# Performance work log

Hardware: AMD Instinct MI355X
Metric: run time of the kernel (lower is better)

## Reference

```python
import jax, jax.numpy as jnp
import numpy as np

N_HEADS, N_LEVELS, N_POINTS = 8, 4, 4
D_MODEL, UNIT = 384, 128

@jax.custom_vjp
def grl(x):
    # Gradient Reversal Layer: identity forward, -grad backward (lambda_=1)
    return x

def _grl_fwd(x):
    return x, None

def _grl_bwd(res, g):
    return (-g,)

grl.defvjp(_grl_fwd, _grl_bwd)


def ms_deform_attn_core(value, spatial_shapes_np, loc, attn):
    """Multi-scale deformable attention (grid_sample bilinear, zeros padding, align_corners=False).
    value: (N, Len_in, nH, hd)   loc: (N, Lq, nH, nL, nP, 2) normalized [0,1]   attn: (N, Lq, nH, nL, nP)
    """
    N, Lq, nH, nL, nP, _ = loc.shape
    hd = value.shape[-1]
    b = jnp.arange(N).reshape(N, 1, 1, 1)
    h = jnp.arange(nH).reshape(1, 1, nH, 1)
    out = jnp.zeros((N, Lq, nH, hd), dtype=value.dtype)
    start = 0
    for l in range(nL):
        H, W = int(spatial_shapes_np[l, 0]), int(spatial_shapes_np[l, 1])
        v = value[:, start:start + H * W]  # (N, H*W, nH, hd)
        start += H * W
        # align_corners=False pixel coords
        x = loc[:, :, :, l, :, 0] * W - 0.5
        y = loc[:, :, :, l, :, 1] * H - 0.5
        x0f, y0f = jnp.floor(x), jnp.floor(y)
        lx, ly = x - x0f, y - y0f
        x0, y0 = x0f.astype(jnp.int32), y0f.astype(jnp.int32)
        def gather(xi, yi):
            valid = ((xi >= 0) & (xi < W) & (yi >= 0) & (yi < H)).astype(value.dtype)
            flat = jnp.clip(yi, 0, H - 1) * W + jnp.clip(xi, 0, W - 1)  # (N,Lq,nH,nP)
            return v[b, flat, h] * valid[..., None]  # (N,Lq,nH,nP,hd)
        s = (((1 - lx) * (1 - ly))[..., None] * gather(x0, y0)
             + (lx * (1 - ly))[..., None] * gather(x0 + 1, y0)
             + ((1 - lx) * ly)[..., None] * gather(x0, y0 + 1)
             + (lx * ly)[..., None] * gather(x0 + 1, y0 + 1))
        out = out + jnp.sum(s * attn[:, :, :, l, :, None], axis=3)
    return out.reshape(N, Lq, nH * hd)


def setup_inputs() -> dict:
    key = jax.random.key(0)
    ks = jax.random.split(key, 12)
    N, Lq = 2, 5440
    spatial = np.array([[64, 64], [32, 32], [16, 16], [8, 8]], dtype=np.int32)
    sizes = spatial[:, 0] * spatial[:, 1]
    Len_in = int(sizes.sum())  # 5440
    lsi = np.concatenate([[0], np.cumsum(sizes)[:-1]]).astype(np.int32)
    D, U, nH, nL, nP = D_MODEL, UNIT, N_HEADS, N_LEVELS, N_POINTS
    def lin(k, fin, fout):
        return jax.random.normal(k, (fin, fout), jnp.float32) / np.sqrt(fin)
    # faithful grid-init bias for sampling offsets
    thetas = np.arange(nH) * (2.0 * np.pi / nH)
    grid = np.stack([np.cos(thetas), np.sin(thetas)], -1)
    grid = grid / np.abs(grid).max(-1, keepdims=True)
    grid = np.tile(grid.reshape(nH, 1, 1, 2), (1, nL, nP, 1))
    for i in range(nP):
        grid[:, :, i, :] *= (i + 1)
    return {
        "query": jax.random.normal(ks[0], (N, Lq, D), jnp.float32),
        "reference_points": jax.random.uniform(ks[1], (N, Lq, nL, 2), jnp.float32),
        "input_flatten": jax.random.normal(ks[2], (N, Len_in, D), jnp.float32),
        "input_spatial_shapes": jnp.asarray(spatial),
        "input_level_start_index": jnp.asarray(lsi),
        "W_off": 0.01 * jax.random.normal(ks[3], (2 * U, nH * nL * nP * 2), jnp.float32),
        "b_off": jnp.asarray(grid.reshape(-1), dtype=jnp.float32),
        "W_attn": lin(ks[4], 2 * U, nH * nL * nP),
        "b_attn": jnp.zeros((nH * nL * nP,), jnp.float32),
        "W_val": lin(ks[5], 2 * U, 3 * U),
        "b_val": jnp.zeros((3 * U,), jnp.float32),
        "W_out": lin(ks[6], 3 * U, 2 * U),
        "b_out": jnp.zeros((2 * U,), jnp.float32),
        "W_attn_zd": lin(ks[7], 3 * U, nH * nL * nP),
        "b_attn_zd": jnp.zeros((nH * nL * nP,), jnp.float32),
        "W_val_zd": lin(ks[8], D, D),
        "b_val_zd": jnp.zeros((D,), jnp.float32),
        "W_out_zd": lin(ks[9], D, U),
        "b_out_zd": jnp.zeros((U,), jnp.float32),
    }


def reference(query, reference_points, input_flatten, input_spatial_shapes, input_level_start_index,
              W_off, b_off, W_attn, b_attn, W_val, b_val, W_out, b_out,
              W_attn_zd, b_attn_zd, W_val_zd, b_val_zd, W_out_zd, b_out_zd):
    N, Lq, _ = query.shape
    nH, nL, nP, U = N_HEADS, N_LEVELS, N_POINTS, UNIT
    ss = np.asarray(input_spatial_shapes)  # static level shapes
    sample_query = query[..., :2 * U]
    off = (sample_query @ W_off + b_off).reshape(N, Lq, nH, nL, nP, 2)
    # offset normalizer = [W_l, H_l] per level
    norm = jnp.asarray(np.stack([ss[:, 1], ss[:, 0]], -1), dtype=query.dtype)
    loc = reference_points[:, :, None, :, None, :] + off / norm[None, None, None, :, None, :]
    # top (content) path
    top_val = (input_flatten[..., :2 * U] @ W_val + b_val).reshape(N, -1, nH, 3 * U // nH)
    aw = jax.nn.softmax((sample_query @ W_attn + b_attn).reshape(N, Lq, nH, nL * nP), -1)
    aw = aw.reshape(N, Lq, nH, nL, nP)
    top_out = ms_deform_attn_core(top_val, ss, loc, aw) @ W_out + b_out
    # bottom (domain) path with gradient reversal on content slice
    bot_val_in = jnp.concatenate([grl(input_flatten[..., :2 * U]), input_flatten[..., 2 * U:]], -1)
    bot_val = (bot_val_in @ W_val_zd + b_val_zd).reshape(N, -1, nH, D_MODEL // nH)
    bot_query = jnp.concatenate([grl(query[..., :2 * U]), query[..., 2 * U:]], -1)
    aw_zd = jax.nn.softmax((bot_query @ W_attn_zd + b_attn_zd).reshape(N, Lq, nH, nL * nP), -1)
    aw_zd = aw_zd.reshape(N, Lq, nH, nL, nP)
    bot_out = ms_deform_attn_core(bot_val, ss, loc, aw_zd) @ W_out_zd + b_out_zd
    return jnp.concatenate([top_out, bot_out], -1)
```

## Files before the change

### kernel.cpp

```cpp
#include <hip/hip_runtime.h>
#include <hip/hip_bf16.h>
#include <math.h>

#define DM   384
#define U2   256
#define HD   48

typedef __attribute__((ext_vector_type(8))) short short8;
typedef __attribute__((ext_vector_type(4))) float floatx4;
typedef __attribute__((ext_vector_type(2))) float floatx2;

static __device__ __forceinline__ unsigned short f2bfbits(float f) {
    __hip_bfloat16 h = __float2bfloat16(f);
    return *reinterpret_cast<unsigned short*>(&h);
}
static __device__ __forceinline__ unsigned pack2(float x, float y) {
    return (unsigned)f2bfbits(x) | ((unsigned)f2bfbits(y) << 16);
}
static __device__ __forceinline__ float bflo(unsigned u) { return __uint_as_float(u << 16); }
static __device__ __forceinline__ float bfhi(unsigned u) { return __uint_as_float(u & 0xffff0000u); }

struct PrepParams {
    const float* q; const float* f;
    __hip_bfloat16 *q_bf, *f_bf;
    const float* wsrc[7]; __hip_bfloat16* wdst[7];
    int K[7], N[7], off[8];
    int nQ4, nF4, total;
};
__global__ __launch_bounds__(256) void prep_kernel(PrepParams d) {
    const int idx = blockIdx.x * 256 + threadIdx.x;
    if (idx >= d.total) return;
    if (idx < d.nQ4) {
        const int i4 = idx * 4;
        const float4 v = *(const float4*)&d.q[i4];
        uint2 pk; pk.x = pack2(v.x, v.y); pk.y = pack2(v.z, v.w);
        *(uint2*)&d.q_bf[i4] = pk;
        return;
    }
    if (idx < d.nQ4 + d.nF4) {
        const int i4 = (idx - d.nQ4) * 4;
        const float4 v = *(const float4*)&d.f[i4];
        uint2 pk; pk.x = pack2(v.x, v.y); pk.y = pack2(v.z, v.w);
        *(uint2*)&d.f_bf[i4] = pk;
        return;
    }
    const int iw = idx - d.nQ4 - d.nF4;
    int s = 0;
#pragma unroll
    for (int i = 1; i < 7; ++i) if (iw >= d.off[i]) s = i;
    const int r = iw - d.off[s];
    const int k = r / d.N[s], n = r - k * d.N[s];
    d.wdst[s][(size_t)n * d.K[s] + k] = __float2bfloat16(d.wsrc[s][r]);
}

struct Seg {
    const __hip_bfloat16* A; int lda;
    const __hip_bfloat16* Bt; int ldbt;
    const float* bias; void* C; int ldc; int K; int omode;
};
struct SegParams { Seg seg[5]; int ystart[5]; int nseg; };

__global__ __launch_bounds__(256) void gemm_seg_kernel(SegParams p) {
    __shared__ __hip_bfloat16 As[64 * 40];
    __shared__ __hip_bfloat16 Bs[64 * 40];

    const int yb = blockIdx.y;
    int s = 0;
#pragma unroll
    for (int i = 1; i < 5; ++i) if (i < p.nseg && yb >= p.ystart[i]) s = i;
    Seg sg;
    switch (s) {
        case 0: sg = p.seg[0]; break;
        case 1: sg = p.seg[1]; break;
        case 2: sg = p.seg[2]; break;
        case 3: sg = p.seg[3]; break;
        default: sg = p.seg[4]; break;
    }
    const int by = yb - p.ystart[s];

    const int t    = threadIdx.x;
    const int bm   = blockIdx.x * 64;
    const int bn   = by * 64;
    const int w    = t >> 6, lane = t & 63;
    const int wm   = (w >> 1) * 32, wn = (w & 1) * 32;
    const int quad = lane >> 4, lm = lane & 15;

    const int r0 = t >> 2, kc = (t & 3) * 8;

    const __hip_bfloat16* Ap = sg.A  + (size_t)(bm + r0) * sg.lda  + kc;
    const __hip_bfloat16* Bp = sg.Bt + (size_t)(bn + r0) * sg.ldbt + kc;

    short8 abf = *(const short8*)Ap;
    short8 bbf = *(const short8*)Bp;

    floatx4 acc[2][2] = {};

    for (int k0 = 0; k0 < sg.K; k0 += 32) {
        *(short8*)&As[r0 * 40 + kc] = abf;
        *(short8*)&Bs[r0 * 40 + kc] = bbf;
        __syncthreads();

        const int kn = k0 + 32;
        if (kn < sg.K) {
            abf = *(const short8*)(Ap + kn);
            bbf = *(const short8*)(Bp + kn);
        }

        short8 af[2], bf[2];
#pragma unroll
        for (int i = 0; i < 2; ++i)
            af[i] = *(const short8*)&As[(wm + i * 16 + lm) * 40 + quad * 8];
#pragma unroll
        for (int j = 0; j < 2; ++j)
            bf[j] = *(const short8*)&Bs[(wn + j * 16 + lm) * 40 + quad * 8];
#pragma unroll
        for (int i = 0; i < 2; ++i)
#pragma unroll
            for (int j = 0; j < 2; ++j)
                acc[i][j] = __builtin_amdgcn_mfma_f32_16x16x32_bf16(
                    af[i], bf[j], acc[i][j], 0, 0, 0);
        __syncthreads();
    }

#pragma unroll
    for (int i = 0; i < 2; ++i)
#pragma unroll
        for (int reg = 0; reg < 4; ++reg) {
            const int row = bm + wm + i * 16 + quad * 4 + reg;
#pragma unroll
            for (int j = 0; j < 2; ++j) {
                const int col = bn + wn + j * 16 + lm;
                const float v = acc[i][j][reg] + sg.bias[col];
                if (sg.omode == 0) {
                    ((float*)sg.C)[(size_t)row * sg.ldc + col] = v;
                } else if (sg.omode == 1) {
                    ((__hip_bfloat16*)sg.C)[(size_t)row * sg.ldc + col] = __float2bfloat16(v);
                } else {
                    const int h = col / 48;
                    const size_t idx = (size_t)row * 768 + h * 96 +
                                       ((sg.omode == 3) ? 48 : 0) + (col - h * 48);
                    ((__hip_bfloat16*)sg.C)[idx] = __float2bfloat16(v);
                }
            }
        }
}

#define SPP 524

__global__ __launch_bounds__(192) void sampler_kernel(
    const float* __restrict__ off_buf,
    const float* __restrict__ logit_top,
    const float* __restrict__ logit_bot,
    const float* __restrict__ ref_pts,
    const int*   __restrict__ ss,
    const int*   __restrict__ lsi,
    const __hip_bfloat16* __restrict__ vcomb,
    __hip_bfloat16* __restrict__ core_top,
    __hip_bfloat16* __restrict__ core_bot,
    int Lq, int LenIn)
{
    __shared__ float sA[2][128];
    __shared__ uint2 sP[2][SPP];
    __shared__ float4 sRed[96][2];

    const int bx  = blockIdx.x;
    const int bid = (bx & 1) * Lq + (bx >> 1);
    const int t   = threadIdx.x;

    float gw[4];
    int   gp[4];

    if (t < 128) {
        const int e = t;
        const int l = (e >> 2) & 3;
        const float2 offv = *(const float2*)&off_buf[(size_t)bid * 256 + 2 * e];
        const float rx = ref_pts[(size_t)(bid * 4 + l) * 2 + 0];
        const float ry = ref_pts[(size_t)(bid * 4 + l) * 2 + 1];
        const int H = ss[2 * l], W = ss[2 * l + 1];
        const int start = lsi[l];

        const float x = (rx + offv.x / (float)W) * (float)W - 0.5f;
        const float y = (ry + offv.y / (float)H) * (float)H - 0.5f;
        const float x0f = floorf(x), y0f = floorf(y);
        const float lx = x - x0f, ly = y - y0f;
        const int ix0 = (int)x0f, iy0 = (int)y0f;
        const int ix1 = ix0 + 1,  iy1 = iy0 + 1;

        const float vx0 = (ix0 >= 0 && ix0 < W) ? 1.f : 0.f;
        const float vx1 = (ix1 >= 0 && ix1 < W) ? 1.f : 0.f;
        const float vy0 = (iy0 >= 0 && iy0 < H) ? 1.f : 0.f;
        const float vy1 = (iy1 >= 0 && iy1 < H) ? 1.f : 0.f;
        const int cx0 = min(max(ix0, 0), W - 1);
        const int cx1 = min(max(ix1, 0), W - 1);
        const int cy0 = min(max(iy0, 0), H - 1);
        const int cy1 = min(max(iy1, 0), H - 1);
        const int base = bid / Lq * LenIn + start;

        gp[0] = base + cy0 * W + cx0;
        gp[1] = base + cy0 * W + cx1;
        gp[2] = base + cy1 * W + cx0;
        gp[3] = base + cy1 * W + cx1;
        gw[0] = (1.f - lx) * (1.f - ly) * vx0 * vy0;
        gw[1] = lx * (1.f - ly) * vx1 * vy0;
        gw[2] = (1.f - lx) * ly * vx0 * vy1;
        gw[3] = lx * ly * vx1 * vy1;
    } else {
        const int lt64 = t - 128;
        const int grp  = lt64 >> 2;
        const int j4   = lt64 & 3;
        const int br   = grp >> 3;
        const int h    = grp & 7;
        const float* L = (br ? logit_bot : logit_top) + (size_t)bid * 128 + h * 16 + j4 * 4;
        const float4 lg = *(const float4*)L;
        float m = fmaxf(fmaxf(lg.x, lg.y), fmaxf(lg.z, lg.w));
        m = fmaxf(m, __shfl_xor(m, 1));
        m = fmaxf(m, __shfl_xor(m, 2));
        float e0 = expf(lg.x - m), e1 = expf(lg.y - m);
        float e2 = expf(lg.z - m), e3 = expf(lg.w - m);
        float sum = e0 + e1 + e2 + e3;
        sum += __shfl_xor(sum, 1);
        sum += __shfl_xor(sum, 2);
        const float inv = 1.f / sum;
        float* dst = &sA[br][h * 16 + j4 * 4];
        dst[0] = e0 * inv; dst[1] = e1 * inv; dst[2] = e2 * inv; dst[3] = e3 * inv;
    }
    __syncthreads();

    if (t < 128) {
        const int e = t;
        const int pidx = 4 * e + (e >> 4);
#pragma unroll
        for (int br = 0; br < 2; ++br) {
            const float a = sA[br][e];
#pragma unroll
            for (int k = 0; k < 4; ++k) {
                uint2 pr;
                pr.x = (unsigned)gp[k];
                pr.y = __float_as_uint(gw[k] * a);
                sP[br][pidx + k] = pr;
            }
        }
    }
    __syncthreads();

    const int half = t / 96;
    const int u    = t - half * 96;
    const int g    = u / 6;
    const int m    = u - g * 6;
    const int br   = g & 1;
    const int h    = g >> 1;

    const uint2* P = sP[br];
    const char* vbase = (const char*)vcomb;
    const unsigned tco = (unsigned)(h * 192 + br * 96 + m * 16);

    floatx2 ac0 = {0.f, 0.f}, ac1 = {0.f, 0.f};
    floatx2 ac2 = {0.f, 0.f}, ac3 = {0.f, 0.f};
    const int lp0 = half * 8;
#pragma unroll
    for (int lp = 0; lp < 8; ++lp) {
        const int ib = 65 * h + 4 * (lp0 + lp);
        uint2 pr[4];
#pragma unroll
        for (int k = 0; k < 4; ++k) pr[k] = P[ib + k];
        uint4 v[4];
#pragma unroll
        for (int k = 0; k < 4; ++k)
            v[k] = *(const uint4*)(vbase + ((pr[k].x & 0x3fffu) * 1536u + tco));
#pragma unroll
        for (int k = 0; k < 4; ++k) {
            const float wv = __uint_as_float(pr[k].y);
            floatx2 wv2 = {wv, wv};
            floatx2 f0 = {bflo(v[k].x), bfhi(v[k].x)};
            floatx2 f1 = {bflo(v[k].y), bfhi(v[k].y)};
            floatx2 f2 = {bflo(v[k].z), bfhi(v[k].z)};
            floatx2 f3 = {bflo(v[k].w), bfhi(v[k].w)};
            ac0 += wv2 * f0;
            ac1 += wv2 * f1;
            ac2 += wv2 * f2;
            ac3 += wv2 * f3;
        }
    }

    if (half) {
        float4 p0; p0.x = ac0.x; p0.y = ac0.y; p0.z = ac1.x; p0.w = ac1.y;
        float4 p1; p1.x = ac2.x; p1.y = ac2.y; p1.z = ac3.x; p1.w = ac3.y;
        sRed[u][0] = p0;
        sRed[u][1] = p1;
    }
    __syncthreads();
    if (!half) {
        const float4 p0 = sRed[u][0];
        const float4 p1 = sRed[u][1];
        uint4 o;
        o.x = pack2(ac0.x + p0.x, ac0.y + p0.y);
        o.y = pack2(ac1.x + p0.z, ac1.y + p0.w);
        o.z = pack2(ac2.x + p1.x, ac2.y + p1.y);
        o.w = pack2(ac3.x + p1.z, ac3.y + p1.w);
        __hip_bfloat16* dst = br ? core_bot : core_top;
        *(uint4*)&dst[(size_t)bid * DM + h * HD + m * 8] = o;
    }
}

extern "C" void kernel_launch(void* const* d_in, const int* in_sizes, int n_in,
                              void* d_out, int out_size, void* d_ws, size_t ws_size,
                              hipStream_t stream) {
    const float* query   = (const float*)d_in[0];
    const float* refpts  = (const float*)d_in[1];
    const float* flat    = (const float*)d_in[2];
    const int*   ss      = (const int*)d_in[3];
    const int*   lsi     = (const int*)d_in[4];
    const float* W_off   = (const float*)d_in[5];
    const float* b_off   = (const float*)d_in[6];
    const float* W_attn  = (const float*)d_in[7];
    const float* b_attn  = (const float*)d_in[8];
    const float* W_val   = (const float*)d_in[9];
    const float* b_val   = (const float*)d_in[10];
    const float* W_out   = (const float*)d_in[11];
    const float* b_out   = (const float*)d_in[12];
    const float* W_attn_zd = (const float*)d_in[13];
    const float* b_attn_zd = (const float*)d_in[14];
    const float* W_val_zd  = (const float*)d_in[15];
    const float* b_val_zd  = (const float*)d_in[16];
    const float* W_out_zd  = (const float*)d_in[17];
    const float* b_out_zd  = (const float*)d_in[18];

    const int Lq    = in_sizes[0] / (2 * DM);
    const int LenIn = in_sizes[2] / (2 * DM);
    const int M  = 2 * Lq;
    const int Mv = 2 * LenIn;

    float* out = (float*)d_out;

    float* ws      = (float*)d_ws;
    float* off_buf = ws;
    float* lt      = off_buf + (size_t)M * 256;
    float* lb      = lt + (size_t)M * 128;
    __hip_bfloat16* q_bf  = (__hip_bfloat16*)(lb + (size_t)M * 128);
    __hip_bfloat16* f_bf  = q_bf + (size_t)M * 384;
    __hip_bfloat16* vcomb = f_bf + (size_t)Mv * 384;
    __hip_bfloat16* ct    = vcomb + (size_t)Mv * 768;
    __hip_bfloat16* cb    = ct + (size_t)M * 384;
    __hip_bfloat16* wtb   = cb + (size_t)M * 384;

    PrepParams pp;
    pp.q = query; pp.f = flat;
    pp.q_bf = q_bf; pp.f_bf = f_bf;
    const float* srcs[7] = {W_attn, W_attn_zd, W_val, W_val_zd, W_out, W_out_zd, W_off};
    const int Ks[7] = {256, 384, 256, 384, 384, 384, 256};
    const int Ns[7] = {128, 128, 384, 384, 256, 128, 256};
    __hip_bfloat16* dsts[7];
    int off = 0;
    for (int i = 0; i < 7; ++i) {
        pp.wsrc[i] = srcs[i]; pp.K[i] = Ks[i]; pp.N[i] = Ns[i];
        pp.off[i] = off;
        dsts[i] = wtb + off;
        pp.wdst[i] = dsts[i];
        off += Ks[i] * Ns[i];
    }
    pp.off[7] = off;
    pp.nQ4 = M * DM / 4;
    pp.nF4 = Mv * DM / 4;
    pp.total = pp.nQ4 + pp.nF4 + off;

    const dim3 blk(256);
    const int mg = M / 64;

    prep_kernel<<<dim3((pp.total + 255) / 256), blk, 0, stream>>>(pp);

    {
        SegParams p;
        p.seg[0] = { q_bf, DM, dsts[6], 256, b_off,     off_buf, 256, 256, 0 };
        p.seg[1] = { q_bf, DM, dsts[0], 256, b_attn,    lt,      128, 256, 0 };
        p.seg[2] = { q_bf, DM, dsts[1], 384, b_attn_zd, lb,      128, 384, 0 };
        p.seg[3] = { f_bf, DM, dsts[2], 256, b_val,     vcomb,   0,   256, 2 };
        p.seg[4] = { f_bf, DM, dsts[3], 384, b_val_zd,  vcomb,   0,   384, 3 };
        p.ystart[0] = 0; p.ystart[1] = 4; p.ystart[2] = 6;
        p.ystart[3] = 8; p.ystart[4] = 14;
        p.nseg = 5;
        gemm_seg_kernel<<<dim3(mg, 20), blk, 0, stream>>>(p);
    }

    sampler_kernel<<<dim3(M), dim3(192), 0, stream>>>(
        off_buf, lt, lb, refpts, ss, lsi, vcomb, ct, cb, Lq, LenIn);

    {
        SegParams p;
        p.seg[0] = { ct, DM, dsts[4], 384, b_out,    out,      DM, 384, 0 };
        p.seg[1] = { cb, DM, dsts[5], 384, b_out_zd, out + U2, DM, 384, 0 };
        p.ystart[0] = 0; p.ystart[1] = 4;
        p.nseg = 2;
        gemm_seg_kernel<<<dim3(mg, 6), blk, 0, stream>>>(p);
    }
}
```

Measured before the change: 221.7 us.

## Fuse fp32-to-bf16 activation conversion into GEMM and pack sampler entries

```diff
diff --git a/kernel.cpp b/kernel.cpp
--- a/kernel.cpp
+++ b/kernel.cpp
@@ -21,30 +21,13 @@
 static __device__ __forceinline__ float bfhi(unsigned u) { return __uint_as_float(u & 0xffff0000u); }
 
 struct PrepParams {
-    const float* q; const float* f;
-    __hip_bfloat16 *q_bf, *f_bf;
     const float* wsrc[7]; __hip_bfloat16* wdst[7];
     int K[7], N[7], off[8];
-    int nQ4, nF4, total;
+    int total;
 };
 __global__ __launch_bounds__(256) void prep_kernel(PrepParams d) {
-    const int idx = blockIdx.x * 256 + threadIdx.x;
-    if (idx >= d.total) return;
-    if (idx < d.nQ4) {
-        const int i4 = idx * 4;
-        const float4 v = *(const float4*)&d.q[i4];
-        uint2 pk; pk.x = pack2(v.x, v.y); pk.y = pack2(v.z, v.w);
-        *(uint2*)&d.q_bf[i4] = pk;
-        return;
-    }
-    if (idx < d.nQ4 + d.nF4) {
-        const int i4 = (idx - d.nQ4) * 4;
-        const float4 v = *(const float4*)&d.f[i4];
-        uint2 pk; pk.x = pack2(v.x, v.y); pk.y = pack2(v.z, v.w);
-        *(uint2*)&d.f_bf[i4] = pk;
-        return;
-    }
-    const int iw = idx - d.nQ4 - d.nF4;
+    const int iw = blockIdx.x * 256 + threadIdx.x;
+    if (iw >= d.total) return;
     int s = 0;
 #pragma unroll
     for (int i = 1; i < 7; ++i) if (iw >= d.off[i]) s = i;
@@ -54,12 +37,13 @@
 }
 
 struct Seg {
-    const __hip_bfloat16* A; int lda;
+    const void* A; int lda;
     const __hip_bfloat16* Bt; int ldbt;
     const float* bias; void* C; int ldc; int K; int omode;
 };
 struct SegParams { Seg seg[5]; int ystart[5]; int nseg; };
 
+template<bool AF32>
 __global__ __launch_bounds__(256) void gemm_seg_kernel(SegParams p) {
     __shared__ __hip_bfloat16 As[64 * 40];
     __shared__ __hip_bfloat16 Bs[64 * 40];
@@ -87,22 +71,42 @@
 
     const int r0 = t >> 2, kc = (t & 3) * 8;
 
-    const __hip_bfloat16* Ap = sg.A  + (size_t)(bm + r0) * sg.lda  + kc;
-    const __hip_bfloat16* Bp = sg.Bt + (size_t)(bn + r0) * sg.ldbt + kc;
-
-    short8 abf = *(const short8*)Ap;
+    const float*          Apf = (const float*)sg.A          + (size_t)(bm + r0) * sg.lda + kc;
+    const __hip_bfloat16* Aph = (const __hip_bfloat16*)sg.A + (size_t)(bm + r0) * sg.lda + kc;
+    const __hip_bfloat16* Bp  = sg.Bt + (size_t)(bn + r0) * sg.ldbt + kc;
+
+    float4 a0, a1;
+    short8 abf;
+    if (AF32) {
+        a0 = *(const float4*)Apf;
+        a1 = *(const float4*)(Apf + 4);
+    } else {
+        abf = *(const short8*)Aph;
+    }
     short8 bbf = *(const short8*)Bp;
 
     floatx4 acc[2][2] = {};
 
     for (int k0 = 0; k0 < sg.K; k0 += 32) {
-        *(short8*)&As[r0 * 40 + kc] = abf;
+        if (AF32) {
+            uint4 pk;
+            pk.x = pack2(a0.x, a0.y); pk.y = pack2(a0.z, a0.w);
+            pk.z = pack2(a1.x, a1.y); pk.w = pack2(a1.z, a1.w);
+            *(uint4*)&As[r0 * 40 + kc] = pk;
+        } else {
+            *(short8*)&As[r0 * 40 + kc] = abf;
+        }
         *(short8*)&Bs[r0 * 40 + kc] = bbf;
         __syncthreads();
 
         const int kn = k0 + 32;
         if (kn < sg.K) {
-            abf = *(const short8*)(Ap + kn);
+            if (AF32) {
+                a0 = *(const float4*)(Apf + kn);
+                a1 = *(const float4*)(Apf + kn + 4);
+            } else {
+                abf = *(const short8*)(Aph + kn);
+            }
             bbf = *(const short8*)(Bp + kn);
         }
 
@@ -159,9 +163,9 @@
     __hip_bfloat16* __restrict__ core_bot,
     int Lq, int LenIn)
 {
-    __shared__ float sA[2][128];
-    __shared__ uint2 sP[2][SPP];
-    __shared__ float4 sRed[96][2];
+    __shared__ float    sA[2][128];
+    __shared__ unsigned sP[2][SPP];
+    __shared__ float4   sRed[96][2];
 
     const int bx  = blockIdx.x;
     const int bid = (bx & 1) * Lq + (bx >> 1);
@@ -234,10 +238,8 @@
             const float a = sA[br][e];
 #pragma unroll
             for (int k = 0; k < 4; ++k) {
-                uint2 pr;
-                pr.x = (unsigned)gp[k];
-                pr.y = __float_as_uint(gw[k] * a);
-                sP[br][pidx + k] = pr;
+                sP[br][pidx + k] =
+                    ((unsigned)f2bfbits(gw[k] * a) << 16) | (unsigned)gp[k];
             }
         }
     }
@@ -250,7 +252,7 @@
     const int br   = g & 1;
     const int h    = g >> 1;
 
-    const uint2* P = sP[br];
+    const unsigned* P = sP[br];
     const char* vbase = (const char*)vcomb;
     const unsigned tco = (unsigned)(h * 192 + br * 96 + m * 16);
 
@@ -260,21 +262,17 @@
 #pragma unroll
     for (int lp = 0; lp < 8; ++lp) {
         const int ib = 65 * h + 4 * (lp0 + lp);
-        uint2 pr[4];
-#pragma unroll
-        for (int k = 0; k < 4; ++k) pr[k] = P[ib + k];
-        uint4 v[4];
-#pragma unroll
-        for (int k = 0; k < 4; ++k)
-            v[k] = *(const uint4*)(vbase + ((pr[k].x & 0x3fffu) * 1536u + tco));
 #pragma unroll
         for (int k = 0; k < 4; ++k) {
-            const float wv = __uint_as_float(pr[k].y);
+            const unsigned uu = P[ib + k];
+            const float wv = __uint_as_float(uu & 0xffff0000u);
+            const unsigned off = (uu & 0x3fffu) * 1536u + tco;
+            const uint4 v = *(const uint4*)(vbase + off);
             floatx2 wv2 = {wv, wv};
-            floatx2 f0 = {bflo(v[k].x), bfhi(v[k].x)};
-            floatx2 f1 = {bflo(v[k].y), bfhi(v[k].y)};
-            floatx2 f2 = {bflo(v[k].z), bfhi(v[k].z)};
-            floatx2 f3 = {bflo(v[k].w), bfhi(v[k].w)};
+            floatx2 f0 = {bflo(v.x), bfhi(v.x)};
+            floatx2 f1 = {bflo(v.y), bfhi(v.y)};
+            floatx2 f2 = {bflo(v.z), bfhi(v.z)};
+            floatx2 f3 = {bflo(v.w), bfhi(v.w)};
             ac0 += wv2 * f0;
             ac1 += wv2 * f1;
             ac2 += wv2 * f2;
@@ -336,16 +334,12 @@
     float* off_buf = ws;
     float* lt      = off_buf + (size_t)M * 256;
     float* lb      = lt + (size_t)M * 128;
-    __hip_bfloat16* q_bf  = (__hip_bfloat16*)(lb + (size_t)M * 128);
-    __hip_bfloat16* f_bf  = q_bf + (size_t)M * 384;
-    __hip_bfloat16* vcomb = f_bf + (size_t)Mv * 384;
+    __hip_bfloat16* vcomb = (__hip_bfloat16*)(lb + (size_t)M * 128);
     __hip_bfloat16* ct    = vcomb + (size_t)Mv * 768;
     __hip_bfloat16* cb    = ct + (size_t)M * 384;
     __hip_bfloat16* wtb   = cb + (size_t)M * 384;
 
     PrepParams pp;
-    pp.q = query; pp.f = flat;
-    pp.q_bf = q_bf; pp.f_bf = f_bf;
     const float* srcs[7] = {W_attn, W_attn_zd, W_val, W_val_zd, W_out, W_out_zd, W_off};
     const int Ks[7] = {256, 384, 256, 384, 384, 384, 256};
     const int Ns[7] = {128, 128, 384, 384, 256, 128, 256};
@@ -359,9 +353,7 @@
         off += Ks[i] * Ns[i];
     }
     pp.off[7] = off;
-    pp.nQ4 = M * DM / 4;
-    pp.nF4 = Mv * DM / 4;
-    pp.total = pp.nQ4 + pp.nF4 + off;
+    pp.total = off;
 
     const dim3 blk(256);
     const int mg = M / 64;
@@ -370,15 +362,15 @@
 
     {
         SegParams p;
-        p.seg[0] = { q_bf, DM, dsts[6], 256, b_off,     off_buf, 256, 256, 0 };
-        p.seg[1] = { q_bf, DM, dsts[0], 256, b_attn,    lt,      128, 256, 0 };
-        p.seg[2] = { q_bf, DM, dsts[1], 384, b_attn_zd, lb,      128, 384, 0 };
-        p.seg[3] = { f_bf, DM, dsts[2], 256, b_val,     vcomb,   0,   256, 2 };
-        p.seg[4] = { f_bf, DM, dsts[3], 384, b_val_zd,  vcomb,   0,   384, 3 };
+        p.seg[0] = { query, DM, dsts[6], 256, b_off,     off_buf, 256, 256, 0 };
+        p.seg[1] = { query, DM, dsts[0], 256, b_attn,    lt,      128, 256, 0 };
+        p.seg[2] = { query, DM, dsts[1], 384, b_attn_zd, lb,      128, 384, 0 };
+        p.seg[3] = { flat,  DM, dsts[2], 256, b_val,     vcomb,   0,   256, 2 };
+        p.seg[4] = { flat,  DM, dsts[3], 384, b_val_zd,  vcomb,   0,   384, 3 };
         p.ystart[0] = 0; p.ystart[1] = 4; p.ystart[2] = 6;
         p.ystart[3] = 8; p.ystart[4] = 14;
         p.nseg = 5;
-        gemm_seg_kernel<<<dim3(mg, 20), blk, 0, stream>>>(p);
+        gemm_seg_kernel<true><<<dim3(mg, 20), blk, 0, stream>>>(p);
     }
 
     sampler_kernel<<<dim3(M), dim3(192), 0, stream>>>(
@@ -390,6 +382,6 @@
         p.seg[1] = { cb, DM, dsts[5], 384, b_out_zd, out + U2, DM, 384, 0 };
         p.ystart[0] = 0; p.ystart[1] = 4;
         p.nseg = 2;
-        gemm_seg_kernel<<<dim3(mg, 6), blk, 0, stream>>>(p);
-    }
-}
+        gemm_seg_kernel<false><<<dim3(mg, 6), blk, 0, stream>>>(p);
+    }
+}
```

New measurement: 226.4 us. 1.02x slower.

## Swizzle GEMM blocks across XCDs and pack sampler weight/index into one word

Applied to the files above, without the earlier changes.

```diff
diff --git a/kernel.cpp b/kernel.cpp
--- a/kernel.cpp
+++ b/kernel.cpp
@@ -58,16 +58,22 @@
     const __hip_bfloat16* Bt; int ldbt;
     const float* bias; void* C; int ldc; int K; int omode;
 };
-struct SegParams { Seg seg[5]; int ystart[5]; int nseg; };
+struct SegParams { Seg seg[5]; int ystart[5]; int nseg; int ny; };
 
 __global__ __launch_bounds__(256) void gemm_seg_kernel(SegParams p) {
     __shared__ __hip_bfloat16 As[64 * 40];
     __shared__ __hip_bfloat16 Bs[64 * 40];
 
-    const int yb = blockIdx.y;
+    const int nb = gridDim.x;
+    const int q8 = nb >> 3, r8 = nb & 7;
+    const int c  = blockIdx.x & 7;
+    const int i  = c * q8 + min(c, r8) + (blockIdx.x >> 3);
+    const int bxi = i / p.ny;
+    const int yb  = i - bxi * p.ny;
+
     int s = 0;
 #pragma unroll
-    for (int i = 1; i < 5; ++i) if (i < p.nseg && yb >= p.ystart[i]) s = i;
+    for (int k = 1; k < 5; ++k) if (k < p.nseg && yb >= p.ystart[k]) s = k;
     Seg sg;
     switch (s) {
         case 0: sg = p.seg[0]; break;
@@ -79,7 +85,7 @@
     const int by = yb - p.ystart[s];
 
     const int t    = threadIdx.x;
-    const int bm   = blockIdx.x * 64;
+    const int bm   = bxi * 64;
     const int bn   = by * 64;
     const int w    = t >> 6, lane = t & 63;
     const int wm   = (w >> 1) * 32, wn = (w & 1) * 32;
@@ -108,29 +114,29 @@
 
         short8 af[2], bf[2];
 #pragma unroll
-        for (int i = 0; i < 2; ++i)
-            af[i] = *(const short8*)&As[(wm + i * 16 + lm) * 40 + quad * 8];
+        for (int ii = 0; ii < 2; ++ii)
+            af[ii] = *(const short8*)&As[(wm + ii * 16 + lm) * 40 + quad * 8];
 #pragma unroll
         for (int j = 0; j < 2; ++j)
             bf[j] = *(const short8*)&Bs[(wn + j * 16 + lm) * 40 + quad * 8];
 #pragma unroll
-        for (int i = 0; i < 2; ++i)
+        for (int ii = 0; ii < 2; ++ii)
 #pragma unroll
             for (int j = 0; j < 2; ++j)
-                acc[i][j] = __builtin_amdgcn_mfma_f32_16x16x32_bf16(
-                    af[i], bf[j], acc[i][j], 0, 0, 0);
+                acc[ii][j] = __builtin_amdgcn_mfma_f32_16x16x32_bf16(
+                    af[ii], bf[j], acc[ii][j], 0, 0, 0);
         __syncthreads();
     }
 
 #pragma unroll
-    for (int i = 0; i < 2; ++i)
+    for (int ii = 0; ii < 2; ++ii)
 #pragma unroll
         for (int reg = 0; reg < 4; ++reg) {
-            const int row = bm + wm + i * 16 + quad * 4 + reg;
+            const int row = bm + wm + ii * 16 + quad * 4 + reg;
 #pragma unroll
             for (int j = 0; j < 2; ++j) {
                 const int col = bn + wn + j * 16 + lm;
-                const float v = acc[i][j][reg] + sg.bias[col];
+                const float v = acc[ii][j][reg] + sg.bias[col];
                 if (sg.omode == 0) {
                     ((float*)sg.C)[(size_t)row * sg.ldc + col] = v;
                 } else if (sg.omode == 1) {
@@ -159,9 +165,9 @@
     __hip_bfloat16* __restrict__ core_bot,
     int Lq, int LenIn)
 {
-    __shared__ float sA[2][128];
-    __shared__ uint2 sP[2][SPP];
-    __shared__ float4 sRed[96][2];
+    __shared__ float    sA[2][128];
+    __shared__ unsigned sP[2][SPP];
+    __shared__ float4   sRed[96][2];
 
     const int bx  = blockIdx.x;
     const int bid = (bx & 1) * Lq + (bx >> 1);
@@ -234,10 +240,8 @@
             const float a = sA[br][e];
 #pragma unroll
             for (int k = 0; k < 4; ++k) {
-                uint2 pr;
-                pr.x = (unsigned)gp[k];
-                pr.y = __float_as_uint(gw[k] * a);
-                sP[br][pidx + k] = pr;
+                sP[br][pidx + k] =
+                    ((unsigned)f2bfbits(gw[k] * a) << 16) | (unsigned)gp[k];
             }
         }
     }
@@ -250,7 +254,7 @@
     const int br   = g & 1;
     const int h    = g >> 1;
 
-    const uint2* P = sP[br];
+    const unsigned* P = sP[br];
     const char* vbase = (const char*)vcomb;
     const unsigned tco = (unsigned)(h * 192 + br * 96 + m * 16);
 
@@ -260,21 +264,17 @@
 #pragma unroll
     for (int lp = 0; lp < 8; ++lp) {
         const int ib = 65 * h + 4 * (lp0 + lp);
-        uint2 pr[4];
-#pragma unroll
-        for (int k = 0; k < 4; ++k) pr[k] = P[ib + k];
-        uint4 v[4];
-#pragma unroll
-        for (int k = 0; k < 4; ++k)
-            v[k] = *(const uint4*)(vbase + ((pr[k].x & 0x3fffu) * 1536u + tco));
 #pragma unroll
         for (int k = 0; k < 4; ++k) {
-            const float wv = __uint_as_float(pr[k].y);
+            const unsigned uu = P[ib + k];
+            const float wv = __uint_as_float(uu & 0xffff0000u);
+            const unsigned off = (uu & 0x3fffu) * 1536u + tco;
+            const uint4 v = *(const uint4*)(vbase + off);
             floatx2 wv2 = {wv, wv};
-            floatx2 f0 = {bflo(v[k].x), bfhi(v[k].x)};
-            floatx2 f1 = {bflo(v[k].y), bfhi(v[k].y)};
-            floatx2 f2 = {bflo(v[k].z), bfhi(v[k].z)};
-            floatx2 f3 = {bflo(v[k].w), bfhi(v[k].w)};
+            floatx2 f0 = {bflo(v.x), bfhi(v.x)};
+            floatx2 f1 = {bflo(v.y), bfhi(v.y)};
+            floatx2 f2 = {bflo(v.z), bfhi(v.z)};
+            floatx2 f3 = {bflo(v.w), bfhi(v.w)};
             ac0 += wv2 * f0;
             ac1 += wv2 * f1;
             ac2 += wv2 * f2;
@@ -377,8 +377,8 @@
         p.seg[4] = { f_bf, DM, dsts[3], 384, b_val_zd,  vcomb,   0,   384, 3 };
         p.ystart[0] = 0; p.ystart[1] = 4; p.ystart[2] = 6;
         p.ystart[3] = 8; p.ystart[4] = 14;
-        p.nseg = 5;
-        gemm_seg_kernel<<<dim3(mg, 20), blk, 0, stream>>>(p);
+        p.nseg = 5; p.ny = 20;
+        gemm_seg_kernel<<<dim3(mg * 20), blk, 0, stream>>>(p);
     }
 
     sampler_kernel<<<dim3(M), dim3(192), 0, stream>>>(
@@ -389,7 +389,7 @@
         p.seg[0] = { ct, DM, dsts[4], 384, b_out,    out,      DM, 384, 0 };
         p.seg[1] = { cb, DM, dsts[5], 384, b_out_zd, out + U2, DM, 384, 0 };
         p.ystart[0] = 0; p.ystart[1] = 4;
-        p.nseg = 2;
-        gemm_seg_kernel<<<dim3(mg, 6), blk, 0, stream>>>(p);
-    }
-}
+        p.nseg = 2; p.ny = 6;
+        gemm_seg_kernel<<<dim3(mg * 6), blk, 0, stream>>>(p);
+    }
+}
```

Result: faster. 213.6 us (median of 2 runs) (-3.6%).
